# Performance work log

Measured on AMD Instinct MI355X. Metric: run time of the kernel, lower is better.

Reference implementation:

```python
import jax, jax.numpy as jnp
import numpy as np

SIGMA = 5.0            # isotropic, voxel_size = 1 -> sigma_voxel == sigma
TRUNCATE = 3.0         # scipy gaussian_filter default truncate used in source
LABELS = (1, 2, 3, 4, 5, 6, 7, 8)
SHAPE = (128, 128, 128)
# upper-triangle entries of the 3x3 second-moment matrix, in the source's
# sorted order: diagonal (00,11,22) first, then off-diagonals (01,12,02)
XS = np.array([0, 1, 2, 0, 1, 0])
YS = np.array([0, 1, 2, 1, 2, 2])


def _gauss_kernel(sigma):
    r = int(TRUNCATE * sigma + 0.5)
    x = np.arange(-r, r + 1, dtype=np.float32)
    k = np.exp(-0.5 * (x / sigma) ** 2)
    k /= k.sum()
    return jnp.asarray(k, dtype=jnp.float32), r


def _blur_axis(arr, kernel, r, axis):
    # separable 1D convolution along `axis` with zero ('constant', cval=0) padding
    arr = jnp.moveaxis(arr, axis, -1)
    shp = arr.shape
    x = arr.reshape(-1, 1, shp[-1])                      # (N, 1, L)
    out = jax.lax.conv_general_dilated(x, kernel.reshape(1, 1, -1), (1,), [(r, r)])
    return jnp.moveaxis(out.reshape(shp), -1, axis)


def gaussian_blur3d(arr, sigma):
    k, r = _gauss_kernel(sigma)
    for ax in (-3, -2, -1):
        arr = _blur_axis(arr, k, r, ax)
    return arr


def setup_inputs() -> dict:
    key = jax.random.key(0)
    segmentation = jax.random.randint(key, SHAPE, 0, 9, dtype=jnp.int32)
    grid = jnp.meshgrid(*(jnp.arange(s, dtype=jnp.float32) for s in SHAPE), indexing='ij')
    coords = jnp.stack(grid)                              # (3, D, H, W) world coordinates
    return {"segmentation": segmentation, "coords": coords}


def _lsd(segmentation, coords):
    xs = jnp.asarray(XS)
    ys = jnp.asarray(YS)
    acc = jnp.zeros((10,) + SHAPE, dtype=jnp.float32)
    for label in LABELS:                                  # small fixed label set
        mask = (segmentation == label).astype(jnp.float32)        # (D,H,W)
        mc = coords * mask                                        # masked coords (3,...)
        outer = mc[xs] * mc[ys]                                   # unique 2nd moments (6,...)
        stack = jnp.concatenate([mask[None], mc, outer], axis=0)  # (10, D, H, W)
        agg = gaussian_blur3d(stack, SIGMA)                       # fused: one blur for all stats
        mass = agg[0]
        denom = jnp.where(mass > 0, mass, 1.0)                    # safe; invalid voxels masked out below
        com = agg[1:4] / denom                                    # center of mass (3,...)
        # mean offset, normalized by max_distance = sigma, mapped to [0,1]
        mean_offset = ((com - coords) / SIGMA * 0.5 + 0.5) * mask
        cov = (agg[4:10] / denom - com[xs] * com[ys]) / (SIGMA * SIGMA)
        desc = jnp.concatenate([mean_offset, cov, mass[None]], axis=0)
        acc = acc + desc * mask[None]                             # descriptors[mask] += descriptor[mask]
    return jnp.clip(acc, 0.0, 1.0)


def reference(segmentation, coords):
    return _lsd(segmentation, coords)
```

## Files before the change

### kernel.cpp

```cpp
#include <hip/hip_runtime.h>
#include <hip/hip_bf16.h>
#include <math.h>


constexpr int NV = 128 * 128 * 128;
constexpr int SLICE = 128 * 128;
constexpr int R = 15;
constexpr int KL = 31;
constexpr int CSTRIDE = 160;
constexpr int RSTRIDE = 6 * CSTRIDE + 8;
constexpr int LCAP = 512;

struct Kw { float k0[KL]; float k1[KL]; float k2[KL]; };

__device__ __forceinline__ void fma4(float4& a, float w, const float4& b) {
    a.x = fmaf(w, b.x, a.x); a.y = fmaf(w, b.y, a.y);
    a.z = fmaf(w, b.z, a.z); a.w = fmaf(w, b.w, a.w);
}

__device__ __forceinline__ float4 load_mask4(const unsigned char* p, int lab) {
    unsigned int u = *(const unsigned int*)p;
    return make_float4(((u       ) & 255u) == (unsigned)lab ? 1.f : 0.f,
                       ((u >>  8 ) & 255u) == (unsigned)lab ? 1.f : 0.f,
                       ((u >> 16 ) & 255u) == (unsigned)lab ? 1.f : 0.f,
                       ((u >> 24 ) & 255u) == (unsigned)lab ? 1.f : 0.f);
}
__device__ __forceinline__ float4 load_mask4(const int* p, int lab) {
    int4 s = *(const int4*)p;
    return make_float4(s.x == lab ? 1.f : 0.f, s.y == lab ? 1.f : 0.f,
                       s.z == lab ? 1.f : 0.f, s.w == lab ? 1.f : 0.f);
}

__device__ __forceinline__ unsigned seg_pack4(const unsigned char* p) {
    return *(const unsigned int*)p;
}
__device__ __forceinline__ unsigned seg_pack4(const int* p) {
    int4 v = *(const int4*)p;
    return (unsigned)(v.x & 255) | ((unsigned)(v.y & 255) << 8) |
           ((unsigned)(v.z & 255) << 16) | ((unsigned)(v.w & 255) << 24);
}

__device__ __forceinline__ float bf_ld(const unsigned short* p) {
    return __uint_as_float(((unsigned int)(*p)) << 16);
}

__device__ __forceinline__ float4 bf4_to_f4(uint2 u) {
    return make_float4(__uint_as_float(u.x << 16),
                       __uint_as_float(u.x & 0xFFFF0000u),
                       __uint_as_float(u.y << 16),
                       __uint_as_float(u.y & 0xFFFF0000u));
}

__device__ __forceinline__ unsigned pack_bf2(float a, float b) {
    __hip_bfloat162 h = __float22bfloat162_rn(make_float2(a, b));
    return *reinterpret_cast<unsigned*>(&h);
}

template <typename ST>
__global__ __launch_bounds__(256) void pass_z_t(const ST* __restrict__ seg,
                                                unsigned short* __restrict__ A,
                                                int label0, size_t a_stride,
                                                Kw kw) {
    __shared__ float kp[3][37];
    if (threadIdx.x < 37) {
        int i = threadIdx.x, j = i - 3; bool ok = (j >= 0) && (j < KL);
        kp[0][i] = ok ? kw.k0[j] : 0.f;
        kp[1][i] = ok ? kw.k1[j] : 0.f;
        kp[2][i] = ok ? kw.k2[j] : 0.f;
    }
    __syncthreads();
    const int label = label0 + blockIdx.y;
    unsigned short* Ab = A + (size_t)blockIdx.y * a_stride;
    const int h = blockIdx.x, g = h & 7, l = h >> 3;
    const int tx = threadIdx.x & 31, ty = threadIdx.x >> 5;
    const int x0 = tx * 4;
    const int z0 = 16 * g + 4 * (l & 3);
    const int y  = (l >> 2) * 8 + ty;

    float4 acc[4][3];
#pragma unroll
    for (int t = 0; t < 4; ++t)
#pragma unroll
        for (int c = 0; c < 3; ++c) acc[t][c] = make_float4(0.f, 0.f, 0.f, 0.f);

    float4 cm = make_float4(0.f, 0.f, 0.f, 0.f), nm = cm;
    {
        int zz = z0 - R;
        if ((unsigned)zz < 128u)
            cm = load_mask4(seg + (zz * SLICE + y * 128 + x0), label);
        int zn = z0 + 1 - R;
        if ((unsigned)zn < 128u)
            nm = load_mask4(seg + (zn * SLICE + y * 128 + x0), label);
    }
    for (int j = 0; j < 34; ++j) {
        float4 fm = make_float4(0.f, 0.f, 0.f, 0.f);
        int zz = z0 + j + 2 - R;
        if (j < 32 && (unsigned)zz < 128u)
            fm = load_mask4(seg + (zz * SLICE + y * 128 + x0), label);
#pragma unroll
        for (int t = 0; t < 4; ++t) {
            int i = j - t + 3;
            fma4(acc[t][0], kp[0][i], cm);
            fma4(acc[t][1], kp[1][i], cm);
            fma4(acc[t][2], kp[2][i], cm);
        }
        cm = nm; nm = fm;
    }
#pragma unroll
    for (int t = 0; t < 4; ++t) {
        int base = (z0 + t) * SLICE + y * 128 + x0;
#pragma unroll
        for (int c = 0; c < 3; ++c) {
            float4 v = acc[t][c];
            uint2 pv = make_uint2(pack_bf2(v.x, v.y), pack_bf2(v.z, v.w));
            *reinterpret_cast<uint2*>(Ab + (size_t)c * NV + base) = pv;
        }
    }
}

__device__ __forceinline__ void do_voxel(const unsigned short* __restrict__ Bu,
                                         int rr, int x, int z0, int y0,
                                         float* __restrict__ out, const Kw& kw) {
    const unsigned short* row = Bu + rr * RSTRIDE + (x + 1);
    float g000 = 0, g001 = 0, g002 = 0, g010 = 0, g011 = 0,
          g020 = 0, g100 = 0, g101 = 0, g110 = 0, g200 = 0;
#pragma unroll
    for (int j = 0; j < KL; ++j) {
        float w0 = kw.k0[j], w1 = kw.k1[j], w2 = kw.k2[j];
        float b0 = bf_ld(row + 0 * CSTRIDE + j);
        float b1 = bf_ld(row + 1 * CSTRIDE + j);
        float b2 = bf_ld(row + 2 * CSTRIDE + j);
        float b3 = bf_ld(row + 3 * CSTRIDE + j);
        float b4 = bf_ld(row + 4 * CSTRIDE + j);
        float b5 = bf_ld(row + 5 * CSTRIDE + j);
        g000 = fmaf(w0, b0, g000); g001 = fmaf(w1, b0, g001); g002 = fmaf(w2, b0, g002);
        g010 = fmaf(w0, b1, g010); g011 = fmaf(w1, b1, g011);
        g020 = fmaf(w0, b2, g020);
        g100 = fmaf(w0, b3, g100); g101 = fmaf(w1, b3, g101);
        g110 = fmaf(w0, b4, g110);
        g200 = fmaf(w0, b5, g200);
    }
    const int z2 = z0 + (rr >> 2), y2 = y0 + (rr & 3);
    const int v = (z2 * 128 + y2) * 128 + x;
    float mass = g000;
    float denom = (mass > 0.f) ? mass : 1.f;
    float inv = 1.f / denom;
    float p = g100 * inv, q = g010 * inv, s = g001 * inv;
    const float cs = 1.0f / 25.0f;
    float o[10];
    o[0] = 0.5f - 0.1f * p;
    o[1] = 0.5f - 0.1f * q;
    o[2] = 0.5f - 0.1f * s;
    o[3] = (g200 * inv - p * p) * cs;
    o[4] = (g020 * inv - q * q) * cs;
    o[5] = (g002 * inv - s * s) * cs;
    o[6] = (g110 * inv - p * q) * cs;
    o[7] = (g011 * inv - q * s) * cs;
    o[8] = (g101 * inv - p * s) * cs;
    o[9] = mass;
#pragma unroll
    for (int c = 0; c < 10; ++c) {
        float val = fminf(fmaxf(o[c], 0.f), 1.f);
        out[(size_t)c * NV + v] = val;
    }
}

__device__ __forceinline__ void zero_voxel(int rr, int x, int z0, int y0,
                                           float* __restrict__ out) {
    const int z2 = z0 + (rr >> 2), y2 = y0 + (rr & 3);
    const int v = (z2 * 128 + y2) * 128 + x;
#pragma unroll
    for (int c = 0; c < 10; ++c) out[(size_t)c * NV + v] = 0.f;
}

template <typename ST>
__global__ __launch_bounds__(128) void pass_yx(const unsigned short* __restrict__ A,
                                               const ST* __restrict__ seg,
                                               float* __restrict__ out,
                                               int label0, size_t a_stride,
                                               Kw kw) {
    __shared__ float kp[3][37];
    __shared__ __align__(16) unsigned short Bu[16 * RSTRIDE];
    __shared__ unsigned short lst[LCAP];
    __shared__ int cnt;

    {
        uint4 z4 = make_uint4(0, 0, 0, 0);
        uint4* b4 = (uint4*)Bu;
        for (int i = threadIdx.x; i < 1936; i += 128) b4[i] = z4;
    }
    if (threadIdx.x < 37) {
        int i = threadIdx.x, j = i - 3; bool ok = (j >= 0) && (j < KL);
        kp[0][i] = ok ? kw.k0[j] : 0.f;
        kp[1][i] = ok ? kw.k1[j] : 0.f;
        kp[2][i] = ok ? kw.k2[j] : 0.f;
    }
    if (threadIdx.x == 0) cnt = 0;
    __syncthreads();

    const int labi = blockIdx.y;
    const int label = label0 + labi;
    const unsigned short* Ab = A + (size_t)labi * a_stride;
    const int h = blockIdx.x, g = h & 7, l = h >> 3;
    const int tx = threadIdx.x & 31, tz = threadIdx.x >> 5;
    const int x0 = tx * 4;
    const int z0 = 16 * g + 4 * (l & 3);
    const int y0 = (l >> 2) * 4;
    const int zs = (z0 + tz) * SLICE;

    const int rr_c = threadIdx.x >> 3, q0_c = threadIdx.x & 7;
    const int vrow_c = ((z0 + (rr_c >> 2)) * 128 + (y0 + (rr_c & 3))) * 128;
    unsigned pk[4];
#pragma unroll
    for (int k = 0; k < 4; ++k)
        pk[k] = seg_pack4(seg + vrow_c + 4 * (q0_c + 8 * k));

    float4 acc[6][4];
#pragma unroll
    for (int c = 0; c < 6; ++c)
#pragma unroll
        for (int t = 0; t < 4; ++t) acc[c][t] = make_float4(0.f, 0.f, 0.f, 0.f);

    uint2 c0 = make_uint2(0u, 0u), c1 = c0, c2 = c0;
    uint2 n0 = c0, n1 = c0, n2 = c0;
    {
        int yy = y0 - R;
        if ((unsigned)yy < 128u) {
            int base = zs + yy * 128 + x0;
            c0 = *(const uint2*)(Ab + base);
            c1 = *(const uint2*)(Ab + NV + base);
            c2 = *(const uint2*)(Ab + 2 * NV + base);
        }
        int yn = y0 + 1 - R;
        if ((unsigned)yn < 128u) {
            int base = zs + yn * 128 + x0;
            n0 = *(const uint2*)(Ab + base);
            n1 = *(const uint2*)(Ab + NV + base);
            n2 = *(const uint2*)(Ab + 2 * NV + base);
        }
    }
    for (int j = 0; j < 34; ++j) {
        uint2 f0 = make_uint2(0u, 0u), f1 = f0, f2 = f0;
        int yy = y0 + j + 2 - R;
        if (j < 32 && (unsigned)yy < 128u) {
            int base = zs + yy * 128 + x0;
            f0 = *(const uint2*)(Ab + base);
            f1 = *(const uint2*)(Ab + NV + base);
            f2 = *(const uint2*)(Ab + 2 * NV + base);
        }
        float4 a0 = bf4_to_f4(c0), a1 = bf4_to_f4(c1), a2 = bf4_to_f4(c2);
#pragma unroll
        for (int t = 0; t < 4; ++t) {
            int i = j - t + 3;
            float w0 = kp[0][i], w1 = kp[1][i], w2 = kp[2][i];
            fma4(acc[0][t], w0, a0);
            fma4(acc[1][t], w1, a0);
            fma4(acc[2][t], w2, a0);
            fma4(acc[3][t], w0, a1);
            fma4(acc[4][t], w1, a1);
            fma4(acc[5][t], w0, a2);
        }
        c0 = n0; c1 = n1; c2 = n2;
        n0 = f0; n1 = f1; n2 = f2;
    }
#pragma unroll
    for (int t = 0; t < 4; ++t) {
        const int row = tz * 4 + t;
#pragma unroll
        for (int c = 0; c < 6; ++c) {
            uint2 pv = make_uint2(pack_bf2(acc[c][t].x, acc[c][t].y),
                                  pack_bf2(acc[c][t].z, acc[c][t].w));
            *reinterpret_cast<uint2*>(Bu + row * RSTRIDE + c * CSTRIDE + 16 + x0) = pv;
        }
    }

    {
        const int lane = threadIdx.x & 63;
        const unsigned long long below_mask = (1ull << lane) - 1ull;
#pragma unroll
        for (int k = 0; k < 4; ++k) {
            const unsigned w = pk[k];
#pragma unroll
            for (int t = 0; t < 4; ++t) {
                const int sv = (int)((w >> (8 * t)) & 255u);
                const int x = 4 * (q0_c + 8 * k) + t;
                const bool mt = (sv == label);
                const bool zt = !mt && (sv < 1 || sv > 8) &&
                                (((x & 7) + 1) == label);
                const bool pred = mt | zt;
                unsigned long long b = __ballot(pred);
                int base = 0;
                if (lane == 0 && b)
                    base = atomicAdd(&cnt, __popcll(b));
                base = __shfl(base, 0);
                if (pred) {
                    int pos = base + __popcll(b & below_mask);
                    if (pos < LCAP)
                        lst[pos] = (unsigned short)((rr_c << 7) | x |
                                                    (zt ? 0x8000 : 0));
                }
            }
        }
    }

    __syncthreads();

    const int total = cnt;
    if (total <= LCAP) {
        for (int e = threadIdx.x; e < total; e += 128) {
            int ent = lst[e];
            int rr = (ent >> 7) & 15, x = ent & 127;
            if (ent & 0x8000) zero_voxel(rr, x, z0, y0, out);
            else do_voxel(Bu, rr, x, z0, y0, out, kw);
        }
    } else {
        for (int e = threadIdx.x; e < 2048; e += 128) {
            int rr = e >> 7, x = e & 127;
            int z2 = z0 + (rr >> 2), y2 = y0 + (rr & 3);
            int sv = (int)seg[(z2 * 128 + y2) * 128 + x] & 255;
            if (sv == label)
                do_voxel(Bu, rr, x, z0, y0, out, kw);
            else if ((sv < 1 || sv > 8) && (((x & 7) + 1) == label))
                zero_voxel(rr, x, z0, y0, out);
        }
    }
}

__global__ __launch_bounds__(256) void seg_to_u8(const int* __restrict__ seg,
                                                 unsigned char* __restrict__ seg8) {
    const int t = blockIdx.x * 256 + threadIdx.x;
    const int4 s = ((const int4*)seg)[t];
    ((uchar4*)seg8)[t] = make_uchar4((unsigned char)s.x, (unsigned char)s.y,
                                     (unsigned char)s.z, (unsigned char)s.w);
}

extern "C" void kernel_launch(void* const* d_in, const int* in_sizes, int n_in,
                              void* d_out, int out_size, void* d_ws, size_t ws_size,
                              hipStream_t stream) {
    const int* seg = (const int*)d_in[0];
    float* out = (float*)d_out;
    unsigned short* A = (unsigned short*)d_ws;
    const size_t AVOL = (size_t)3 * NV;

    Kw kw;
    double gg[KL], S = 0.0;
    for (int j = 0; j < KL; ++j) { double d = j - R; gg[j] = exp(-0.5 * d * d / 25.0); S += gg[j]; }
    for (int j = 0; j < KL; ++j) {
        double gn = gg[j] / S, d = j - R;
        kw.k0[j] = (float)gn;
        kw.k1[j] = (float)(-d * gn);
        kw.k2[j] = (float)(d * d * gn);
    }


    const size_t need_all = 8 * AVOL * sizeof(unsigned short) + NV;
    const size_t need_one = AVOL * sizeof(unsigned short) + NV;

    if (ws_size >= need_all) {
        unsigned char* seg8 = (unsigned char*)d_ws + 8 * AVOL * sizeof(unsigned short);
        seg_to_u8<<<dim3(2048), dim3(256), 0, stream>>>(seg, seg8);
        pass_z_t<unsigned char><<<dim3(512, 8), dim3(256), 0, stream>>>(
            seg8, A, 1, AVOL, kw);
        pass_yx<unsigned char><<<dim3(1024, 8), dim3(128), 0, stream>>>(
            A, seg8, out, 1, AVOL, kw);
    } else if (ws_size >= need_one) {
        unsigned char* seg8 = (unsigned char*)d_ws + AVOL * sizeof(unsigned short);
        seg_to_u8<<<dim3(2048), dim3(256), 0, stream>>>(seg, seg8);
        for (int label = 1; label <= 8; ++label) {
            pass_z_t<unsigned char><<<dim3(512, 1), dim3(256), 0, stream>>>(
                seg8, A, label, 0, kw);
            pass_yx<unsigned char><<<dim3(1024, 1), dim3(128), 0, stream>>>(
                A, seg8, out, label, 0, kw);
        }
    } else {
        for (int label = 1; label <= 8; ++label) {
            pass_z_t<int><<<dim3(512, 1), dim3(256), 0, stream>>>(
                seg, A, label, 0, kw);
            pass_yx<int><<<dim3(1024, 1), dim3(128), 0, stream>>>(
                A, seg, out, label, 0, kw);
        }
    }
}
```

Baseline: 407.5 us.

## Fuse per-label yx pass into single kernel looping labels with smem output staging

Replaces the per-label grid of pass_yx with one kernel where each block owns a 2x4x128 voxel tile and loops over all 8 labels. Results for the tile build up in shared memory as fp16 and are written to the output once, coalesced, at the end. This removes scattered per-label output writes and the explicit zeroing of voxels whose value is outside the label set. The staging adds fp16 rounding of outputs, more serialized work per block with a barrier on every label, and relies on every voxel being initialized to zero in shared memory.

```diff
diff --git a/kernel.cpp b/kernel.cpp
--- a/kernel.cpp
+++ b/kernel.cpp
@@ -1,5 +1,6 @@
 #include <hip/hip_runtime.h>
 #include <hip/hip_bf16.h>
+#include <hip/hip_fp16.h>
 #include <math.h>
 
 
@@ -118,9 +119,9 @@
     }
 }
 
-__device__ __forceinline__ void do_voxel(const unsigned short* __restrict__ Bu,
-                                         int rr, int x, int z0, int y0,
-                                         float* __restrict__ out, const Kw& kw) {
+__device__ __forceinline__ void conv_voxel(const unsigned short* __restrict__ Bu,
+                                           int rr, int x, const Kw& kw,
+                                           float o[10]) {
     const unsigned short* row = Bu + rr * RSTRIDE + (x + 1);
     float g000 = 0, g001 = 0, g002 = 0, g010 = 0, g011 = 0,
           g020 = 0, g100 = 0, g101 = 0, g110 = 0, g200 = 0;
@@ -140,14 +141,11 @@
         g110 = fmaf(w0, b4, g110);
         g200 = fmaf(w0, b5, g200);
     }
-    const int z2 = z0 + (rr >> 2), y2 = y0 + (rr & 3);
-    const int v = (z2 * 128 + y2) * 128 + x;
     float mass = g000;
     float denom = (mass > 0.f) ? mass : 1.f;
     float inv = 1.f / denom;
     float p = g100 * inv, q = g010 * inv, s = g001 * inv;
     const float cs = 1.0f / 25.0f;
-    float o[10];
     o[0] = 0.5f - 0.1f * p;
     o[1] = 0.5f - 0.1f * q;
     o[2] = 0.5f - 0.1f * s;
@@ -159,10 +157,18 @@
     o[8] = (g101 * inv - p * s) * cs;
     o[9] = mass;
 #pragma unroll
-    for (int c = 0; c < 10; ++c) {
-        float val = fminf(fmaxf(o[c], 0.f), 1.f);
-        out[(size_t)c * NV + v] = val;
-    }
+    for (int c = 0; c < 10; ++c) o[c] = fminf(fmaxf(o[c], 0.f), 1.f);
+}
+
+__device__ __forceinline__ void do_voxel_out(const unsigned short* __restrict__ Bu,
+                                             int rr, int x, int z0, int y0,
+                                             float* __restrict__ out, const Kw& kw) {
+    float o[10];
+    conv_voxel(Bu, rr, x, kw, o);
+    const int z2 = z0 + (rr >> 2), y2 = y0 + (rr & 3);
+    const int v = (z2 * 128 + y2) * 128 + x;
+#pragma unroll
+    for (int c = 0; c < 10; ++c) out[(size_t)c * NV + v] = o[c];
 }
 
 __device__ __forceinline__ void zero_voxel(int rr, int x, int z0, int y0,
@@ -171,6 +177,193 @@
     const int v = (z2 * 128 + y2) * 128 + x;
 #pragma unroll
     for (int c = 0; c < 10; ++c) out[(size_t)c * NV + v] = 0.f;
+}
+
+template <typename ST>
+__global__ __launch_bounds__(256, 4) void pass_yx_all(
+        const unsigned short* __restrict__ A,
+        const ST* __restrict__ seg,
+        float* __restrict__ out,
+        size_t a_stride, Kw kw) {
+    __shared__ float4 kq4[40];
+    __shared__ __align__(16) unsigned short Bu[8 * RSTRIDE];
+    __shared__ __align__(16) unsigned stage32[1024 * 5];
+    __shared__ unsigned short lst[LCAP];
+    __shared__ int cnt2[2];
+
+    {
+        uint4 z4 = make_uint4(0, 0, 0, 0);
+        uint4* b4 = (uint4*)Bu;
+        for (int i = threadIdx.x; i < 968; i += 256) b4[i] = z4;
+        uint4* s4 = (uint4*)stage32;
+        for (int i = threadIdx.x; i < 1280; i += 256) s4[i] = z4;
+    }
+    if (threadIdx.x < 40) {
+        int i = threadIdx.x, j = i - 3; bool ok = (j >= 0) && (j < KL);
+        kq4[i] = make_float4(ok ? kw.k0[j] : 0.f, ok ? kw.k1[j] : 0.f,
+                             ok ? kw.k2[j] : 0.f, 0.f);
+    }
+    if (threadIdx.x == 0) { cnt2[0] = 0; cnt2[1] = 0; }
+
+    const int b = blockIdx.x, g = b & 7, l = b >> 3;
+    const int z0 = 16 * g + 2 * (l & 7);
+    const int y0 = (l >> 3) * 4;
+
+    const unsigned pk = seg_pack4(seg +
+        ((z0 + (threadIdx.x >> 7)) * 128 + (y0 + ((threadIdx.x >> 5) & 3))) * 128 +
+        (threadIdx.x & 31) * 4);
+
+    const int w = threadIdx.x >> 6;
+    const int zr = w & 1, cg = w >> 1;
+    const int lane = threadIdx.x & 63;
+    const int lx = lane & 31, lh = lane >> 5;
+    const int x0 = 4 * lx;
+    const int t0 = 2 * lh;
+    const int zrs = (z0 + zr) * SLICE;
+    const unsigned long long below_mask = (1ull << lane) - 1ull;
+
+    __syncthreads();
+
+    for (int labi = 0; labi < 8; ++labi) {
+        const int label = 1 + labi;
+        const unsigned short* Ab0 = A + (size_t)labi * a_stride;
+        const unsigned short* Ab1 = Ab0 + NV;
+        const unsigned short* Ab2 = Ab0 + 2 * NV;
+
+        float4 acc[3][2];
+#pragma unroll
+        for (int c = 0; c < 3; ++c)
+#pragma unroll
+            for (int k = 0; k < 2; ++k) acc[c][k] = make_float4(0.f, 0.f, 0.f, 0.f);
+
+        uint2 u0c = make_uint2(0u, 0u), u0n = u0c;
+        uint2 u1c = u0c, u1n = u0c, u2c = u0c, u2n = u0c;
+        {
+            int yy = y0 - R;
+            if ((unsigned)yy < 128u) {
+                int base = zrs + yy * 128 + x0;
+                if (cg == 0) u0c = *(const uint2*)(Ab0 + base);
+                else { u1c = *(const uint2*)(Ab1 + base); u2c = *(const uint2*)(Ab2 + base); }
+            }
+            int yn = y0 + 1 - R;
+            if ((unsigned)yn < 128u) {
+                int base = zrs + yn * 128 + x0;
+                if (cg == 0) u0n = *(const uint2*)(Ab0 + base);
+                else { u1n = *(const uint2*)(Ab1 + base); u2n = *(const uint2*)(Ab2 + base); }
+            }
+        }
+        for (int j = 0; j < 34; ++j) {
+            uint2 f0 = make_uint2(0u, 0u), f1 = f0, f2 = f0;
+            int yy = y0 + j + 2 - R;
+            if (j < 32 && (unsigned)yy < 128u) {
+                int base = zrs + yy * 128 + x0;
+                if (cg == 0) f0 = *(const uint2*)(Ab0 + base);
+                else { f1 = *(const uint2*)(Ab1 + base); f2 = *(const uint2*)(Ab2 + base); }
+            }
+            if (cg == 0) {
+                float4 a0 = bf4_to_f4(u0c);
+#pragma unroll
+                for (int k = 0; k < 2; ++k) {
+                    float4 wv = kq4[j + 3 - (t0 + k)];
+                    fma4(acc[0][k], wv.x, a0);
+                    fma4(acc[1][k], wv.y, a0);
+                    fma4(acc[2][k], wv.z, a0);
+                }
+            } else {
+                float4 a1 = bf4_to_f4(u1c), a2 = bf4_to_f4(u2c);
+#pragma unroll
+                for (int k = 0; k < 2; ++k) {
+                    float4 wv = kq4[j + 3 - (t0 + k)];
+                    fma4(acc[0][k], wv.x, a1);
+                    fma4(acc[1][k], wv.y, a1);
+                    fma4(acc[2][k], wv.x, a2);
+                }
+            }
+            u0c = u0n; u1c = u1n; u2c = u2n;
+            u0n = f0;  u1n = f1;  u2n = f2;
+        }
+
+        __syncthreads();
+
+#pragma unroll
+        for (int k = 0; k < 2; ++k) {
+            const int row = zr * 4 + t0 + k;
+#pragma unroll
+            for (int c3 = 0; c3 < 3; ++c3) {
+                const int c = cg * 3 + c3;
+                float4 v = acc[c3][k];
+                uint2 pv = make_uint2(pack_bf2(v.x, v.y), pack_bf2(v.z, v.w));
+                *reinterpret_cast<uint2*>(Bu + row * RSTRIDE + c * CSTRIDE + 16 + x0) = pv;
+            }
+        }
+        {
+            int* cw = &cnt2[labi & 1];
+#pragma unroll
+            for (int t = 0; t < 4; ++t) {
+                const int sv = (int)((pk >> (8 * t)) & 255u);
+                const bool pred = (sv == label);
+                unsigned long long bal = __ballot(pred);
+                int base = 0;
+                if (lane == 0 && bal) base = atomicAdd(cw, (int)__popcll(bal));
+                base = __shfl(base, 0);
+                if (pred) {
+                    int pos = base + (int)__popcll(bal & below_mask);
+                    if (pos < LCAP)
+                        lst[pos] = (unsigned short)(4 * threadIdx.x + t);
+                }
+            }
+            if (threadIdx.x == 0) cnt2[(labi + 1) & 1] = 0;
+        }
+
+        __syncthreads();
+
+        const int total = cnt2[labi & 1];
+        if (total <= LCAP) {
+            for (int e = threadIdx.x; e < total; e += 256) {
+                int ent = lst[e];
+                int rr = ent >> 7, x = ent & 127;
+                float o[10];
+                conv_voxel(Bu, rr, x, kw, o);
+                unsigned* s = stage32 + (rr * 128 + x) * 5;
+#pragma unroll
+                for (int i = 0; i < 5; ++i) {
+                    __half2 hp = __float22half2_rn(make_float2(o[2 * i], o[2 * i + 1]));
+                    s[i] = *reinterpret_cast<unsigned*>(&hp);
+                }
+            }
+        } else {
+#pragma unroll
+            for (int t = 0; t < 4; ++t) {
+                const int sv = (int)((pk >> (8 * t)) & 255u);
+                if (sv == label) {
+                    int vx = 4 * threadIdx.x + t;
+                    int rr = vx >> 7, x = vx & 127;
+                    float o[10];
+                    conv_voxel(Bu, rr, x, kw, o);
+                    unsigned* s = stage32 + vx * 5;
+#pragma unroll
+                    for (int i = 0; i < 5; ++i) {
+                        __half2 hp = __float22half2_rn(make_float2(o[2 * i], o[2 * i + 1]));
+                        s[i] = *reinterpret_cast<unsigned*>(&hp);
+                    }
+                }
+            }
+        }
+    }
+
+    __syncthreads();
+
+    const __half* sh = (const __half*)stage32;
+    for (int c = 0; c < 10; ++c) {
+        float* oc = out + (size_t)c * NV;
+#pragma unroll
+        for (int k = 0; k < 4; ++k) {
+            int idx = threadIdx.x + k * 256;
+            float f = __half2float(sh[idx * 10 + c]);
+            int gb = ((z0 + (idx >> 9)) * 128 + y0) * 128 + (idx & 511);
+            oc[gb] = f;
+        }
+    }
 }
 
 template <typename ST>
@@ -180,13 +373,13 @@
                                                int label0, size_t a_stride,
                                                Kw kw) {
     __shared__ float kp[3][37];
-    __shared__ __align__(16) unsigned short Bu[16 * RSTRIDE];
+    __shared__ __align__(16) unsigned short Bu2[16 * RSTRIDE];
     __shared__ unsigned short lst[LCAP];
     __shared__ int cnt;
 
     {
         uint4 z4 = make_uint4(0, 0, 0, 0);
-        uint4* b4 = (uint4*)Bu;
+        uint4* b4 = (uint4*)Bu2;
         for (int i = threadIdx.x; i < 1936; i += 128) b4[i] = z4;
     }
     if (threadIdx.x < 37) {
@@ -270,7 +463,7 @@
         for (int c = 0; c < 6; ++c) {
             uint2 pv = make_uint2(pack_bf2(acc[c][t].x, acc[c][t].y),
                                   pack_bf2(acc[c][t].z, acc[c][t].w));
-            *reinterpret_cast<uint2*>(Bu + row * RSTRIDE + c * CSTRIDE + 16 + x0) = pv;
+            *reinterpret_cast<uint2*>(Bu2 + row * RSTRIDE + c * CSTRIDE + 16 + x0) = pv;
         }
     }
 
@@ -288,16 +481,14 @@
                 const bool zt = !mt && (sv < 1 || sv > 8) &&
                                 (((x & 7) + 1) == label);
                 const bool pred = mt | zt;
-                unsigned long long b = __ballot(pred);
+                unsigned long long bal = __ballot(pred);
                 int base = 0;
-                if (lane == 0 && b)
-                    base = atomicAdd(&cnt, __popcll(b));
+                if (lane == 0 && bal) base = atomicAdd(&cnt, (int)__popcll(bal));
                 base = __shfl(base, 0);
                 if (pred) {
-                    int pos = base + __popcll(b & below_mask);
+                    int pos = base + (int)__popcll(bal & below_mask);
                     if (pos < LCAP)
-                        lst[pos] = (unsigned short)((rr_c << 7) | x |
-                                                    (zt ? 0x8000 : 0));
+                        lst[pos] = (unsigned short)((rr_c << 7) | x | (zt ? 0x8000 : 0));
                 }
             }
         }
@@ -311,7 +502,7 @@
             int ent = lst[e];
             int rr = (ent >> 7) & 15, x = ent & 127;
             if (ent & 0x8000) zero_voxel(rr, x, z0, y0, out);
-            else do_voxel(Bu, rr, x, z0, y0, out, kw);
+            else do_voxel_out(Bu2, rr, x, z0, y0, out, kw);
         }
     } else {
         for (int e = threadIdx.x; e < 2048; e += 128) {
@@ -319,7 +510,7 @@
             int z2 = z0 + (rr >> 2), y2 = y0 + (rr & 3);
             int sv = (int)seg[(z2 * 128 + y2) * 128 + x] & 255;
             if (sv == label)
-                do_voxel(Bu, rr, x, z0, y0, out, kw);
+                do_voxel_out(Bu2, rr, x, z0, y0, out, kw);
             else if ((sv < 1 || sv > 8) && (((x & 7) + 1) == label))
                 zero_voxel(rr, x, z0, y0, out);
         }
@@ -361,8 +552,8 @@
         seg_to_u8<<<dim3(2048), dim3(256), 0, stream>>>(seg, seg8);
         pass_z_t<unsigned char><<<dim3(512, 8), dim3(256), 0, stream>>>(
             seg8, A, 1, AVOL, kw);
-        pass_yx<unsigned char><<<dim3(1024, 8), dim3(128), 0, stream>>>(
-            A, seg8, out, 1, AVOL, kw);
+        pass_yx_all<unsigned char><<<dim3(2048), dim3(256), 0, stream>>>(
+            A, seg8, out, AVOL, kw);
     } else if (ws_size >= need_one) {
         unsigned char* seg8 = (unsigned char*)d_ws + AVOL * sizeof(unsigned short);
         seg_to_u8<<<dim3(2048), dim3(256), 0, stream>>>(seg, seg8);
```

New measurement: 452.1 us. 1.11x slower.

## Halve yx-pass tile, split channel work across waves, stage segmentation in LDS

Applied to the files above, without the earlier changes.

The y/x blur pass now handles a 2x4 (z,y) row tile per block instead of 4x4, doubling the grid. The two waves in each block split the six moment channels (3 each) rather than each thread computing all six, which halves the per-thread accumulators from 24 to 12 float4. Segmentation labels are staged in shared memory and the kernel weights are packed as float4. The aim is more blocks and lower register pressure for better occupancy, at the cost of less y-halo reuse per block and more redundant loads overall.

```diff
diff --git a/kernel.cpp b/kernel.cpp
--- a/kernel.cpp
+++ b/kernel.cpp
@@ -118,9 +118,9 @@
     }
 }
 
-__device__ __forceinline__ void do_voxel(const unsigned short* __restrict__ Bu,
-                                         int rr, int x, int z0, int y0,
-                                         float* __restrict__ out, const Kw& kw) {
+__device__ __forceinline__ void conv_voxel(const unsigned short* __restrict__ Bu,
+                                           int rr, int x, const Kw& kw,
+                                           float o[10]) {
     const unsigned short* row = Bu + rr * RSTRIDE + (x + 1);
     float g000 = 0, g001 = 0, g002 = 0, g010 = 0, g011 = 0,
           g020 = 0, g100 = 0, g101 = 0, g110 = 0, g200 = 0;
@@ -140,14 +140,11 @@
         g110 = fmaf(w0, b4, g110);
         g200 = fmaf(w0, b5, g200);
     }
-    const int z2 = z0 + (rr >> 2), y2 = y0 + (rr & 3);
-    const int v = (z2 * 128 + y2) * 128 + x;
     float mass = g000;
     float denom = (mass > 0.f) ? mass : 1.f;
     float inv = 1.f / denom;
     float p = g100 * inv, q = g010 * inv, s = g001 * inv;
     const float cs = 1.0f / 25.0f;
-    float o[10];
     o[0] = 0.5f - 0.1f * p;
     o[1] = 0.5f - 0.1f * q;
     o[2] = 0.5f - 0.1f * s;
@@ -159,146 +156,142 @@
     o[8] = (g101 * inv - p * s) * cs;
     o[9] = mass;
 #pragma unroll
-    for (int c = 0; c < 10; ++c) {
-        float val = fminf(fmaxf(o[c], 0.f), 1.f);
-        out[(size_t)c * NV + v] = val;
-    }
-}
-
-__device__ __forceinline__ void zero_voxel(int rr, int x, int z0, int y0,
-                                           float* __restrict__ out) {
-    const int z2 = z0 + (rr >> 2), y2 = y0 + (rr & 3);
-    const int v = (z2 * 128 + y2) * 128 + x;
-#pragma unroll
-    for (int c = 0; c < 10; ++c) out[(size_t)c * NV + v] = 0.f;
+    for (int c = 0; c < 10; ++c) o[c] = fminf(fmaxf(o[c], 0.f), 1.f);
 }
 
 template <typename ST>
-__global__ __launch_bounds__(128) void pass_yx(const unsigned short* __restrict__ A,
-                                               const ST* __restrict__ seg,
-                                               float* __restrict__ out,
-                                               int label0, size_t a_stride,
-                                               Kw kw) {
-    __shared__ float kp[3][37];
-    __shared__ __align__(16) unsigned short Bu[16 * RSTRIDE];
+__global__ __launch_bounds__(128) void pass_yx8(const unsigned short* __restrict__ A,
+                                                const ST* __restrict__ seg,
+                                                float* __restrict__ out,
+                                                int label0, size_t a_stride,
+                                                Kw kw) {
+    __shared__ float4 kq4[40];
+    __shared__ __align__(16) unsigned short Bu[8 * RSTRIDE];
+    __shared__ unsigned seg_l[256];
     __shared__ unsigned short lst[LCAP];
     __shared__ int cnt;
 
     {
         uint4 z4 = make_uint4(0, 0, 0, 0);
         uint4* b4 = (uint4*)Bu;
-        for (int i = threadIdx.x; i < 1936; i += 128) b4[i] = z4;
-    }
-    if (threadIdx.x < 37) {
+        for (int i = threadIdx.x; i < 968; i += 128) b4[i] = z4;
+    }
+    if (threadIdx.x < 40) {
         int i = threadIdx.x, j = i - 3; bool ok = (j >= 0) && (j < KL);
-        kp[0][i] = ok ? kw.k0[j] : 0.f;
-        kp[1][i] = ok ? kw.k1[j] : 0.f;
-        kp[2][i] = ok ? kw.k2[j] : 0.f;
+        kq4[i] = make_float4(ok ? kw.k0[j] : 0.f, ok ? kw.k1[j] : 0.f,
+                             ok ? kw.k2[j] : 0.f, 0.f);
     }
     if (threadIdx.x == 0) cnt = 0;
+
+    const int label = label0 + blockIdx.y;
+    const unsigned short* Ab0 = A + (size_t)blockIdx.y * a_stride;
+    const unsigned short* Ab1 = Ab0 + NV;
+    const unsigned short* Ab2 = Ab0 + 2 * NV;
+
+    const int h = blockIdx.x, g = h & 7, l = h >> 3;
+    const int z0 = 16 * g + 2 * (l & 7);
+    const int y0 = (l >> 3) * 4;
+
+    {
+#pragma unroll
+        for (int q = threadIdx.x; q < 256; q += 128) {
+            const int rr = q >> 5;
+            const int gb = ((z0 + (rr >> 2)) * 128 + (y0 + (rr & 3))) * 128 +
+                           4 * (q & 31);
+            seg_l[q] = seg_pack4(seg + gb);
+        }
+    }
+
+    const int lane = threadIdx.x & 63;
+    const int w = threadIdx.x >> 6;
+    const int lx = lane & 31;
+    const int zr = lane >> 5;
+    const int x0 = 4 * lx;
+    const int zrs = (z0 + zr) * SLICE;
+    const unsigned long long below_mask = (1ull << lane) - 1ull;
+
     __syncthreads();
 
-    const int labi = blockIdx.y;
-    const int label = label0 + labi;
-    const unsigned short* Ab = A + (size_t)labi * a_stride;
-    const int h = blockIdx.x, g = h & 7, l = h >> 3;
-    const int tx = threadIdx.x & 31, tz = threadIdx.x >> 5;
-    const int x0 = tx * 4;
-    const int z0 = 16 * g + 4 * (l & 3);
-    const int y0 = (l >> 2) * 4;
-    const int zs = (z0 + tz) * SLICE;
-
-    const int rr_c = threadIdx.x >> 3, q0_c = threadIdx.x & 7;
-    const int vrow_c = ((z0 + (rr_c >> 2)) * 128 + (y0 + (rr_c & 3))) * 128;
-    unsigned pk[4];
-#pragma unroll
-    for (int k = 0; k < 4; ++k)
-        pk[k] = seg_pack4(seg + vrow_c + 4 * (q0_c + 8 * k));
-
-    float4 acc[6][4];
-#pragma unroll
-    for (int c = 0; c < 6; ++c)
+    float4 acc[3][4];
+#pragma unroll
+    for (int c = 0; c < 3; ++c)
 #pragma unroll
         for (int t = 0; t < 4; ++t) acc[c][t] = make_float4(0.f, 0.f, 0.f, 0.f);
 
-    uint2 c0 = make_uint2(0u, 0u), c1 = c0, c2 = c0;
-    uint2 n0 = c0, n1 = c0, n2 = c0;
+    uint2 c1 = make_uint2(0u, 0u), n1 = c1, f1 = c1;
+    uint2 c2 = c1, n2 = c1, f2 = c1;
     {
         int yy = y0 - R;
         if ((unsigned)yy < 128u) {
-            int base = zs + yy * 128 + x0;
-            c0 = *(const uint2*)(Ab + base);
-            c1 = *(const uint2*)(Ab + NV + base);
-            c2 = *(const uint2*)(Ab + 2 * NV + base);
+            int base = zrs + yy * 128 + x0;
+            if (w == 0) c1 = *(const uint2*)(Ab0 + base);
+            else { c1 = *(const uint2*)(Ab1 + base); c2 = *(const uint2*)(Ab2 + base); }
         }
         int yn = y0 + 1 - R;
         if ((unsigned)yn < 128u) {
-            int base = zs + yn * 128 + x0;
-            n0 = *(const uint2*)(Ab + base);
-            n1 = *(const uint2*)(Ab + NV + base);
-            n2 = *(const uint2*)(Ab + 2 * NV + base);
+            int base = zrs + yn * 128 + x0;
+            if (w == 0) n1 = *(const uint2*)(Ab0 + base);
+            else { n1 = *(const uint2*)(Ab1 + base); n2 = *(const uint2*)(Ab2 + base); }
         }
     }
     for (int j = 0; j < 34; ++j) {
-        uint2 f0 = make_uint2(0u, 0u), f1 = f0, f2 = f0;
+        f1 = make_uint2(0u, 0u); f2 = f1;
         int yy = y0 + j + 2 - R;
         if (j < 32 && (unsigned)yy < 128u) {
-            int base = zs + yy * 128 + x0;
-            f0 = *(const uint2*)(Ab + base);
-            f1 = *(const uint2*)(Ab + NV + base);
-            f2 = *(const uint2*)(Ab + 2 * NV + base);
-        }
-        float4 a0 = bf4_to_f4(c0), a1 = bf4_to_f4(c1), a2 = bf4_to_f4(c2);
-#pragma unroll
-        for (int t = 0; t < 4; ++t) {
-            int i = j - t + 3;
-            float w0 = kp[0][i], w1 = kp[1][i], w2 = kp[2][i];
-            fma4(acc[0][t], w0, a0);
-            fma4(acc[1][t], w1, a0);
-            fma4(acc[2][t], w2, a0);
-            fma4(acc[3][t], w0, a1);
-            fma4(acc[4][t], w1, a1);
-            fma4(acc[5][t], w0, a2);
-        }
-        c0 = n0; c1 = n1; c2 = n2;
-        n0 = f0; n1 = f1; n2 = f2;
-    }
+            int base = zrs + yy * 128 + x0;
+            if (w == 0) f1 = *(const uint2*)(Ab0 + base);
+            else { f1 = *(const uint2*)(Ab1 + base); f2 = *(const uint2*)(Ab2 + base); }
+        }
+        if (w == 0) {
+            float4 a0 = bf4_to_f4(c1);
+#pragma unroll
+            for (int t = 0; t < 4; ++t) {
+                float4 wv = kq4[j + 3 - t];
+                fma4(acc[0][t], wv.x, a0);
+                fma4(acc[1][t], wv.y, a0);
+                fma4(acc[2][t], wv.z, a0);
+            }
+        } else {
+            float4 a1 = bf4_to_f4(c1), a2 = bf4_to_f4(c2);
+#pragma unroll
+            for (int t = 0; t < 4; ++t) {
+                float4 wv = kq4[j + 3 - t];
+                fma4(acc[0][t], wv.x, a1);
+                fma4(acc[1][t], wv.y, a1);
+                fma4(acc[2][t], wv.x, a2);
+            }
+        }
+        c1 = n1; n1 = f1; c2 = n2; n2 = f2;
+    }
+
 #pragma unroll
     for (int t = 0; t < 4; ++t) {
-        const int row = tz * 4 + t;
-#pragma unroll
-        for (int c = 0; c < 6; ++c) {
-            uint2 pv = make_uint2(pack_bf2(acc[c][t].x, acc[c][t].y),
-                                  pack_bf2(acc[c][t].z, acc[c][t].w));
-            *reinterpret_cast<uint2*>(Bu + row * RSTRIDE + c * CSTRIDE + 16 + x0) = pv;
-        }
-    }
-
-    {
-        const int lane = threadIdx.x & 63;
-        const unsigned long long below_mask = (1ull << lane) - 1ull;
-#pragma unroll
-        for (int k = 0; k < 4; ++k) {
-            const unsigned w = pk[k];
-#pragma unroll
-            for (int t = 0; t < 4; ++t) {
-                const int sv = (int)((w >> (8 * t)) & 255u);
-                const int x = 4 * (q0_c + 8 * k) + t;
-                const bool mt = (sv == label);
-                const bool zt = !mt && (sv < 1 || sv > 8) &&
-                                (((x & 7) + 1) == label);
-                const bool pred = mt | zt;
-                unsigned long long b = __ballot(pred);
-                int base = 0;
-                if (lane == 0 && b)
-                    base = atomicAdd(&cnt, __popcll(b));
-                base = __shfl(base, 0);
-                if (pred) {
-                    int pos = base + __popcll(b & below_mask);
-                    if (pos < LCAP)
-                        lst[pos] = (unsigned short)((rr_c << 7) | x |
-                                                    (zt ? 0x8000 : 0));
-                }
+        const int row = zr * 4 + t;
+        const int cb = 3 * w;
+#pragma unroll
+        for (int c3 = 0; c3 < 3; ++c3) {
+            float4 v = acc[c3][t];
+            uint2 pv = make_uint2(pack_bf2(v.x, v.y), pack_bf2(v.z, v.w));
+            *reinterpret_cast<uint2*>(Bu + row * RSTRIDE + (cb + c3) * CSTRIDE + 16 + x0) = pv;
+        }
+    }
+    {
+        const unsigned char* s8 = (const unsigned char*)seg_l;
+#pragma unroll
+        for (int s = 0; s < 8; ++s) {
+            const int v = (w << 9) + (s << 6) + lane;
+            const int sv = (int)s8[v];
+            const bool mt = (sv == label);
+            const bool zt = !mt && (sv < 1 || sv > 8) && (((v & 7) + 1) == label);
+            const bool pred = mt | zt;
+            unsigned long long bal = __ballot(pred);
+            int base = 0;
+            if (lane == 0 && bal) base = atomicAdd(&cnt, (int)__popcll(bal));
+            base = __shfl(base, 0);
+            if (pred) {
+                int pos = base + (int)__popcll(bal & below_mask);
+                if (pos < LCAP)
+                    lst[pos] = (unsigned short)(v | (zt ? 0x8000 : 0));
             }
         }
     }
@@ -309,19 +302,35 @@
     if (total <= LCAP) {
         for (int e = threadIdx.x; e < total; e += 128) {
             int ent = lst[e];
-            int rr = (ent >> 7) & 15, x = ent & 127;
-            if (ent & 0x8000) zero_voxel(rr, x, z0, y0, out);
-            else do_voxel(Bu, rr, x, z0, y0, out, kw);
+            int v = ent & 1023, rr = v >> 7, x = v & 127;
+            const int gb = ((z0 + (rr >> 2)) * 128 + (y0 + (rr & 3))) * 128 + x;
+            if (ent & 0x8000) {
+#pragma unroll
+                for (int c = 0; c < 10; ++c) out[(size_t)c * NV + gb] = 0.f;
+            } else {
+                float o[10];
+                conv_voxel(Bu, rr, x, kw, o);
+#pragma unroll
+                for (int c = 0; c < 10; ++c) out[(size_t)c * NV + gb] = o[c];
+            }
         }
     } else {
-        for (int e = threadIdx.x; e < 2048; e += 128) {
-            int rr = e >> 7, x = e & 127;
-            int z2 = z0 + (rr >> 2), y2 = y0 + (rr & 3);
-            int sv = (int)seg[(z2 * 128 + y2) * 128 + x] & 255;
-            if (sv == label)
-                do_voxel(Bu, rr, x, z0, y0, out, kw);
-            else if ((sv < 1 || sv > 8) && (((x & 7) + 1) == label))
-                zero_voxel(rr, x, z0, y0, out);
+        const unsigned char* s8 = (const unsigned char*)seg_l;
+#pragma unroll
+        for (int k = 0; k < 8; ++k) {
+            const int v = 8 * (int)threadIdx.x + k;
+            const int sv = (int)s8[v];
+            const int rr = v >> 7, x = v & 127;
+            const int gb = ((z0 + (rr >> 2)) * 128 + (y0 + (rr & 3))) * 128 + x;
+            if (sv == label) {
+                float o[10];
+                conv_voxel(Bu, rr, x, kw, o);
+#pragma unroll
+                for (int c = 0; c < 10; ++c) out[(size_t)c * NV + gb] = o[c];
+            } else if ((sv < 1 || sv > 8) && (((v & 7) + 1) == label)) {
+#pragma unroll
+                for (int c = 0; c < 10; ++c) out[(size_t)c * NV + gb] = 0.f;
+            }
         }
     }
 }
@@ -361,7 +370,7 @@
         seg_to_u8<<<dim3(2048), dim3(256), 0, stream>>>(seg, seg8);
         pass_z_t<unsigned char><<<dim3(512, 8), dim3(256), 0, stream>>>(
             seg8, A, 1, AVOL, kw);
-        pass_yx<unsigned char><<<dim3(1024, 8), dim3(128), 0, stream>>>(
+        pass_yx8<unsigned char><<<dim3(2048, 8), dim3(128), 0, stream>>>(
             A, seg8, out, 1, AVOL, kw);
     } else if (ws_size >= need_one) {
         unsigned char* seg8 = (unsigned char*)d_ws + AVOL * sizeof(unsigned short);
@@ -369,14 +378,14 @@
         for (int label = 1; label <= 8; ++label) {
             pass_z_t<unsigned char><<<dim3(512, 1), dim3(256), 0, stream>>>(
                 seg8, A, label, 0, kw);
-            pass_yx<unsigned char><<<dim3(1024, 1), dim3(128), 0, stream>>>(
+            pass_yx8<unsigned char><<<dim3(2048, 1), dim3(128), 0, stream>>>(
                 A, seg8, out, label, 0, kw);
         }
     } else {
         for (int label = 1; label <= 8; ++label) {
             pass_z_t<int><<<dim3(512, 1), dim3(256), 0, stream>>>(
                 seg, A, label, 0, kw);
-            pass_yx<int><<<dim3(1024, 1), dim3(128), 0, stream>>>(
+            pass_yx8<int><<<dim3(2048, 1), dim3(128), 0, stream>>>(
                 A, seg, out, label, 0, kw);
         }
     }
```

Result: slower. 432.7 us (+6.2%).

## Switch intermediates to fp16 and interleave LDS channels per voxel

Applied to the files above, without the earlier changes.

Intermediate blur buffers change from bf16 to fp16. The shared-memory tile moves from channel-planar to voxel-interleaved (six halves per x), so the x-convolution reads three 32-bit words per tap instead of six 16-bit loads. Kernel weights are packed into float4 so each tap needs one LDS load. This cuts LDS instruction count, but fp16 conversion and the narrower range could hurt accuracy on large second-moment values, and the 12-byte stride may cause bank conflicts.

```diff
diff --git a/kernel.cpp b/kernel.cpp
--- a/kernel.cpp
+++ b/kernel.cpp
@@ -1,5 +1,5 @@
 #include <hip/hip_runtime.h>
-#include <hip/hip_bf16.h>
+#include <hip/hip_fp16.h>
 #include <math.h>
 
 
@@ -7,8 +7,8 @@
 constexpr int SLICE = 128 * 128;
 constexpr int R = 15;
 constexpr int KL = 31;
-constexpr int CSTRIDE = 160;
-constexpr int RSTRIDE = 6 * CSTRIDE + 8;
+constexpr int TS = 6;
+constexpr int RSTRIDE = 160 * TS + 8;
 constexpr int LCAP = 512;
 
 struct Kw { float k0[KL]; float k1[KL]; float k2[KL]; };
@@ -40,20 +40,18 @@
            ((unsigned)(v.z & 255) << 16) | ((unsigned)(v.w & 255) << 24);
 }
 
-__device__ __forceinline__ float bf_ld(const unsigned short* p) {
-    return __uint_as_float(((unsigned int)(*p)) << 16);
-}
-
-__device__ __forceinline__ float4 bf4_to_f4(uint2 u) {
-    return make_float4(__uint_as_float(u.x << 16),
-                       __uint_as_float(u.x & 0xFFFF0000u),
-                       __uint_as_float(u.y << 16),
-                       __uint_as_float(u.y & 0xFFFF0000u));
-}
-
-__device__ __forceinline__ unsigned pack_bf2(float a, float b) {
-    __hip_bfloat162 h = __float22bfloat162_rn(make_float2(a, b));
+__device__ __forceinline__ unsigned pack_h2(float a, float b) {
+    __half2 h = __float22half2_rn(make_float2(a, b));
     return *reinterpret_cast<unsigned*>(&h);
+}
+__device__ __forceinline__ float h_lo(unsigned u) {
+    return __half2float(__ushort_as_half((unsigned short)(u & 0xffffu)));
+}
+__device__ __forceinline__ float h_hi(unsigned u) {
+    return __half2float(__ushort_as_half((unsigned short)(u >> 16)));
+}
+__device__ __forceinline__ float4 h4_to_f4(uint2 u) {
+    return make_float4(h_lo(u.x), h_hi(u.x), h_lo(u.y), h_hi(u.y));
 }
 
 template <typename ST>
@@ -112,27 +110,26 @@
 #pragma unroll
         for (int c = 0; c < 3; ++c) {
             float4 v = acc[t][c];
-            uint2 pv = make_uint2(pack_bf2(v.x, v.y), pack_bf2(v.z, v.w));
+            uint2 pv = make_uint2(pack_h2(v.x, v.y), pack_h2(v.z, v.w));
             *reinterpret_cast<uint2*>(Ab + (size_t)c * NV + base) = pv;
         }
     }
 }
 
-__device__ __forceinline__ void do_voxel(const unsigned short* __restrict__ Bu,
-                                         int rr, int x, int z0, int y0,
-                                         float* __restrict__ out, const Kw& kw) {
-    const unsigned short* row = Bu + rr * RSTRIDE + (x + 1);
+__device__ __forceinline__ void conv_voxel(const unsigned short* __restrict__ Bu,
+                                           int rr, int x, const Kw& kw,
+                                           float o[10]) {
+    const unsigned short* row = Bu + rr * RSTRIDE + (x + 1) * TS;
     float g000 = 0, g001 = 0, g002 = 0, g010 = 0, g011 = 0,
           g020 = 0, g100 = 0, g101 = 0, g110 = 0, g200 = 0;
 #pragma unroll
     for (int j = 0; j < KL; ++j) {
+        const unsigned* p = (const unsigned*)(row + TS * j);
+        unsigned ua = p[0], ub = p[1], uc = p[2];
         float w0 = kw.k0[j], w1 = kw.k1[j], w2 = kw.k2[j];
-        float b0 = bf_ld(row + 0 * CSTRIDE + j);
-        float b1 = bf_ld(row + 1 * CSTRIDE + j);
-        float b2 = bf_ld(row + 2 * CSTRIDE + j);
-        float b3 = bf_ld(row + 3 * CSTRIDE + j);
-        float b4 = bf_ld(row + 4 * CSTRIDE + j);
-        float b5 = bf_ld(row + 5 * CSTRIDE + j);
+        float b0 = h_lo(ua), b1 = h_hi(ua);
+        float b2 = h_lo(ub), b3 = h_hi(ub);
+        float b4 = h_lo(uc), b5 = h_hi(uc);
         g000 = fmaf(w0, b0, g000); g001 = fmaf(w1, b0, g001); g002 = fmaf(w2, b0, g002);
         g010 = fmaf(w0, b1, g010); g011 = fmaf(w1, b1, g011);
         g020 = fmaf(w0, b2, g020);
@@ -140,14 +137,11 @@
         g110 = fmaf(w0, b4, g110);
         g200 = fmaf(w0, b5, g200);
     }
-    const int z2 = z0 + (rr >> 2), y2 = y0 + (rr & 3);
-    const int v = (z2 * 128 + y2) * 128 + x;
     float mass = g000;
     float denom = (mass > 0.f) ? mass : 1.f;
     float inv = 1.f / denom;
     float p = g100 * inv, q = g010 * inv, s = g001 * inv;
     const float cs = 1.0f / 25.0f;
-    float o[10];
     o[0] = 0.5f - 0.1f * p;
     o[1] = 0.5f - 0.1f * q;
     o[2] = 0.5f - 0.1f * s;
@@ -159,10 +153,18 @@
     o[8] = (g101 * inv - p * s) * cs;
     o[9] = mass;
 #pragma unroll
-    for (int c = 0; c < 10; ++c) {
-        float val = fminf(fmaxf(o[c], 0.f), 1.f);
-        out[(size_t)c * NV + v] = val;
-    }
+    for (int c = 0; c < 10; ++c) o[c] = fminf(fmaxf(o[c], 0.f), 1.f);
+}
+
+__device__ __forceinline__ void do_voxel_out(const unsigned short* __restrict__ Bu,
+                                             int rr, int x, int z0, int y0,
+                                             float* __restrict__ out, const Kw& kw) {
+    float o[10];
+    conv_voxel(Bu, rr, x, kw, o);
+    const int z2 = z0 + (rr >> 2), y2 = y0 + (rr & 3);
+    const int v = (z2 * 128 + y2) * 128 + x;
+#pragma unroll
+    for (int c = 0; c < 10; ++c) out[(size_t)c * NV + v] = o[c];
 }
 
 __device__ __forceinline__ void zero_voxel(int rr, int x, int z0, int y0,
@@ -179,7 +181,7 @@
                                                float* __restrict__ out,
                                                int label0, size_t a_stride,
                                                Kw kw) {
-    __shared__ float kp[3][37];
+    __shared__ float4 kq4[40];
     __shared__ __align__(16) unsigned short Bu[16 * RSTRIDE];
     __shared__ unsigned short lst[LCAP];
     __shared__ int cnt;
@@ -189,11 +191,10 @@
         uint4* b4 = (uint4*)Bu;
         for (int i = threadIdx.x; i < 1936; i += 128) b4[i] = z4;
     }
-    if (threadIdx.x < 37) {
+    if (threadIdx.x < 40) {
         int i = threadIdx.x, j = i - 3; bool ok = (j >= 0) && (j < KL);
-        kp[0][i] = ok ? kw.k0[j] : 0.f;
-        kp[1][i] = ok ? kw.k1[j] : 0.f;
-        kp[2][i] = ok ? kw.k2[j] : 0.f;
+        kq4[i] = make_float4(ok ? kw.k0[j] : 0.f, ok ? kw.k1[j] : 0.f,
+                             ok ? kw.k2[j] : 0.f, 0.f);
     }
     if (threadIdx.x == 0) cnt = 0;
     __syncthreads();
@@ -248,29 +249,34 @@
             f1 = *(const uint2*)(Ab + NV + base);
             f2 = *(const uint2*)(Ab + 2 * NV + base);
         }
-        float4 a0 = bf4_to_f4(c0), a1 = bf4_to_f4(c1), a2 = bf4_to_f4(c2);
+        float4 a0 = h4_to_f4(c0), a1 = h4_to_f4(c1), a2 = h4_to_f4(c2);
 #pragma unroll
         for (int t = 0; t < 4; ++t) {
-            int i = j - t + 3;
-            float w0 = kp[0][i], w1 = kp[1][i], w2 = kp[2][i];
-            fma4(acc[0][t], w0, a0);
-            fma4(acc[1][t], w1, a0);
-            fma4(acc[2][t], w2, a0);
-            fma4(acc[3][t], w0, a1);
-            fma4(acc[4][t], w1, a1);
-            fma4(acc[5][t], w0, a2);
+            float4 wv = kq4[j + 3 - t];
+            fma4(acc[0][t], wv.x, a0);
+            fma4(acc[1][t], wv.y, a0);
+            fma4(acc[2][t], wv.z, a0);
+            fma4(acc[3][t], wv.x, a1);
+            fma4(acc[4][t], wv.y, a1);
+            fma4(acc[5][t], wv.x, a2);
         }
         c0 = n0; c1 = n1; c2 = n2;
         n0 = f0; n1 = f1; n2 = f2;
     }
+
 #pragma unroll
     for (int t = 0; t < 4; ++t) {
         const int row = tz * 4 + t;
-#pragma unroll
-        for (int c = 0; c < 6; ++c) {
-            uint2 pv = make_uint2(pack_bf2(acc[c][t].x, acc[c][t].y),
-                                  pack_bf2(acc[c][t].z, acc[c][t].w));
-            *reinterpret_cast<uint2*>(Bu + row * RSTRIDE + c * CSTRIDE + 16 + x0) = pv;
+        unsigned short* rbase = Bu + row * RSTRIDE + (16 + x0) * TS;
+#pragma unroll
+        for (int xi = 0; xi < 4; ++xi) {
+            unsigned* w32 = (unsigned*)(rbase + xi * TS);
+            float v0 = (&acc[0][t].x)[xi], v1 = (&acc[1][t].x)[xi];
+            float v2 = (&acc[2][t].x)[xi], v3 = (&acc[3][t].x)[xi];
+            float v4 = (&acc[4][t].x)[xi], v5 = (&acc[5][t].x)[xi];
+            w32[0] = pack_h2(v0, v1);
+            w32[1] = pack_h2(v2, v3);
+            w32[2] = pack_h2(v4, v5);
         }
     }
 
@@ -288,16 +294,14 @@
                 const bool zt = !mt && (sv < 1 || sv > 8) &&
                                 (((x & 7) + 1) == label);
                 const bool pred = mt | zt;
-                unsigned long long b = __ballot(pred);
+                unsigned long long bal = __ballot(pred);
                 int base = 0;
-                if (lane == 0 && b)
-                    base = atomicAdd(&cnt, __popcll(b));
+                if (lane == 0 && bal) base = atomicAdd(&cnt, (int)__popcll(bal));
                 base = __shfl(base, 0);
                 if (pred) {
-                    int pos = base + __popcll(b & below_mask);
+                    int pos = base + (int)__popcll(bal & below_mask);
                     if (pos < LCAP)
-                        lst[pos] = (unsigned short)((rr_c << 7) | x |
-                                                    (zt ? 0x8000 : 0));
+                        lst[pos] = (unsigned short)((rr_c << 7) | x | (zt ? 0x8000 : 0));
                 }
             }
         }
@@ -311,7 +315,7 @@
             int ent = lst[e];
             int rr = (ent >> 7) & 15, x = ent & 127;
             if (ent & 0x8000) zero_voxel(rr, x, z0, y0, out);
-            else do_voxel(Bu, rr, x, z0, y0, out, kw);
+            else do_voxel_out(Bu, rr, x, z0, y0, out, kw);
         }
     } else {
         for (int e = threadIdx.x; e < 2048; e += 128) {
@@ -319,7 +323,7 @@
             int z2 = z0 + (rr >> 2), y2 = y0 + (rr & 3);
             int sv = (int)seg[(z2 * 128 + y2) * 128 + x] & 255;
             if (sv == label)
-                do_voxel(Bu, rr, x, z0, y0, out, kw);
+                do_voxel_out(Bu, rr, x, z0, y0, out, kw);
             else if ((sv < 1 || sv > 8) && (((x & 7) + 1) == label))
                 zero_voxel(rr, x, z0, y0, out);
         }
```

Result: no change. 408.8 us (+0.3%).
